# Kernel optimization log

Measured on AMD Instinct MI355X. Metric: run time of the kernel, lower is better.

## Reference

```python
import jax, jax.numpy as jnp
import numpy as np

EPS = float(np.finfo(np.float32).eps)
H = 256          # hidden_size
K = 10           # num_event_types
B, S = 32, 4096  # batch, seq_len


def _linear_params(kw, kb, fan_in, fan_out):
    # torch nn.Linear default init (uniform +-1/sqrt(fan_in)), then abs + clamp(min=eps)
    bound = 1.0 / np.sqrt(fan_in)
    w = jnp.clip(jnp.abs(jax.random.uniform(kw, (fan_out, fan_in), minval=-bound, maxval=bound, dtype=jnp.float32)), EPS)
    b = jnp.clip(jnp.abs(jax.random.uniform(kb, (fan_out,), minval=-bound, maxval=bound, dtype=jnp.float32)), EPS)
    return w, b


def setup_inputs() -> dict:
    key = jax.random.key(0)
    ks = jax.random.split(key, 12)
    w1, b1 = _linear_params(ks[0], ks[1], 1, H)        # layer_dense_1
    w2, b2 = _linear_params(ks[2], ks[3], 2 * H, H)    # layer_dense_2
    wA, bA = _linear_params(ks[4], ks[5], H, H)        # module_list[0]
    wB, bB = _linear_params(ks[6], ks[7], H, H)        # module_list[1]
    w3, b3 = _linear_params(ks[8], ks[9], H, K)        # layer_dense_3 linear
    hidden_states = jax.random.normal(ks[10], (B, S, H), dtype=jnp.float32)
    time_delta_seqs = jax.random.uniform(ks[11], (B, S), dtype=jnp.float32)
    return dict(hidden_states=hidden_states, time_delta_seqs=time_delta_seqs,
                w1=w1, b1=b1, w2=w2, b2=b2, wA=wA, bA=bA, wB=wB, bB=bB, w3=w3, b3=b3)


def _cumul_hazard(td, h, w1, b1, w2, b2, wA, bA, wB, bB, w3, b3):
    # layer_dense_1: Linear(1 -> H) on td[..., None]
    t = td[..., None] * w1[:, 0] + b1                      # [B,S,H]
    out = jnp.tanh(jnp.concatenate([h, t], axis=-1) @ w2.T + b2)  # [B,S,H]
    out = jnp.tanh(out @ wA.T + bA)
    out = jnp.tanh(out @ wB.T + bB)
    return jax.nn.softplus(out @ w3.T + b3)                # [B,S,K]


def reference(hidden_states, time_delta_seqs, w1, b1, w2, b2, wA, bA, wB, bB, w3, b3):
    f = lambda td: _cumul_hazard(td, hidden_states, w1, b1, w2, b2, wA, bA, wB, bB, w3, b3)
    # Each output element depends only on its own t[b,s] (elementwise in time),
    # so a single forward-mode JVP with tangent=ones yields the exact per-element
    # derivative for ALL event types at once (fuses torch's per-type grad loop).
    integral_lambda, d_dt = jax.jvp(f, (time_delta_seqs,), (jnp.ones_like(time_delta_seqs),))
    # torch takes grad of .mean() over [B,S], which scales the derivative by 1/(B*S)
    derivative_integral_lambda = d_dt / time_delta_seqs.size
    return integral_lambda, derivative_integral_lambda
```

## Files before the change

### kernel.cpp

```cpp
#include <hip/hip_runtime.h>
#include <hip/hip_bf16.h>
#include <stdint.h>

typedef __bf16 bf16x8 __attribute__((ext_vector_type(8)));
typedef __bf16 bf16x4 __attribute__((ext_vector_type(4)));
typedef float  f32x4  __attribute__((ext_vector_type(4)));
typedef float  f32x2  __attribute__((ext_vector_type(2)));

#define MFMA16(a,b,c) __builtin_amdgcn_mfma_f32_16x16x32_bf16((a),(b),(c),0,0,0)

static constexpr int H_   = 256;
static constexpr int KEV  = 10;
static constexpr int NTOK = 32 * 4096;

__device__ __forceinline__ float ptanh(float x){
    float t = x * x;
    float n = fmaf(t, t + 105.0f, 945.0f);
    float d = fmaf(t, fmaf(t, 15.0f, 420.0f), 945.0f);
    float r = x * n * __builtin_amdgcn_rcpf(d);
    return __builtin_amdgcn_fmed3f(r, -1.0f, 1.0f);
}

__device__ __forceinline__ bf16x8 cvtFrag(const float* p){
    f32x4 a = *(const f32x4*)p;
    f32x4 b = *(const f32x4*)(p + 4);
    bf16x8 r;
    #pragma unroll
    for (int j = 0; j < 4; ++j){ r[j] = (__bf16)a[j]; r[4 + j] = (__bf16)b[j]; }
    return r;
}

__global__ void prep_vc(const float* __restrict__ w1, const float* __restrict__ b1,
                        const float* __restrict__ w2, const float* __restrict__ b2,
                        const float* __restrict__ b3, float* __restrict__ vc){
    int j = blockIdx.x * 4 + (threadIdx.x >> 6);
    int l = threadIdx.x & 63;
    const float* row = w2 + (size_t)j * (2 * H_) + H_;
    float v = 0.f, cc = 0.f;
    #pragma unroll
    for (int i = 0; i < 4; ++i){
        int k = l + 64 * i;
        float w = row[k];
        v  += w * w1[k];
        cc += w * b1[k];
    }
    #pragma unroll
    for (int off = 32; off; off >>= 1){
        v  += __shfl_down(v,  off, 64);
        cc += __shfl_down(cc, off, 64);
    }
    if (l == 0){ vc[j] = v; vc[H_ + j] = cc + b2[j]; }
    if (blockIdx.x == 0 && threadIdx.x < 16)
        vc[2 * H_ + threadIdx.x] = (threadIdx.x < KEV) ? b3[threadIdx.x] : 0.0f;
}

__global__ void prep_pack(const float* __restrict__ w2, const float* __restrict__ wA,
                          const float* __restrict__ wB, const float* __restrict__ w3,
                          __hip_bfloat16* __restrict__ pk){
    int b  = blockIdx.x;
    int L  = b >> 4, n0 = b & 15;
    const float* W; int K, nrows;
    if (b == 48){ W = w3; K = H_; nrows = KEV; }
    else { W = (L == 0) ? w2 : ((L == 1) ? wA : wB); K = (L == 0) ? 2 * H_ : H_; nrows = 16; }
    __hip_bfloat16* dst = pk + (size_t)b * 4096;
    int t = threadIdx.x;
    #pragma unroll
    for (int u = 0; u < 2; ++u){
        int slot = t * 2 + u;
        int s = slot >> 6, q = (slot >> 4) & 3, c = slot & 15;
        int rr = (b == 48) ? c : (n0 * 16 + c);
        if (c < nrows){
            const float* src = W + (size_t)rr * K + 32 * s + 8 * q;
            #pragma unroll
            for (int j = 0; j < 8; ++j) dst[slot * 8 + j] = __float2bfloat16(src[j]);
        } else {
            #pragma unroll
            for (int j = 0; j < 8; ++j) dst[slot * 8 + j] = __float2bfloat16(0.0f);
        }
    }
}

typedef const __attribute__((address_space(1))) void* gvp;
typedef __attribute__((address_space(3)))       void* lvp;

__device__ __forceinline__ void stage_chunk(const __hip_bfloat16* wpk, __hip_bfloat16* buf,
                                            int g, int wave, int lane){
    const char* src = (const char*)wpk + (size_t)g * 8192 + wave * 2048 + lane * 16;
    char*       dst = (char*)buf + wave * 2048;
    __builtin_amdgcn_global_load_lds((gvp)(const void*)src,          (lvp)(void*)dst,          16, 0, 0);
    __builtin_amdgcn_global_load_lds((gvp)(const void*)(src + 1024), (lvp)(void*)(dst + 1024), 16, 0, 0);
}

__global__ __launch_bounds__(256, 2) void chfn_kernel(
    const float* __restrict__ hs, const float* __restrict__ td,
    const __hip_bfloat16* __restrict__ wpk,
    const float* __restrict__ bA, const float* __restrict__ bB,
    const float* __restrict__ vc,
    float* __restrict__ out)
{
    __shared__ __hip_bfloat16 sW[2 * 4096];
    __shared__ __hip_bfloat16 sA[4 * 16 * H_];
    __shared__ __hip_bfloat16 sD[4 * 16 * H_];

    const int tid  = threadIdx.x;
    const int wave = tid >> 6;
    const int lane = tid & 63;
    const int q    = lane >> 4;
    const int c    = lane & 15;
    const int tb   = blockIdx.x * 64 + wave * 16;
    const int wrow = wave * 16;
    const int xr   = (c >> 1) & 7;
    const int ws   = q * 16 + c;

    stage_chunk(wpk, sW, 0, wave, lane);

    bf16x8 aF[8], aB[8];
    {
        const float* h0 = hs + (size_t)(tb + c) * H_ + 8 * q;
        #pragma unroll
        for (int s = 0; s < 8; ++s) aF[s] = cvtFrag(h0 + 32 * s);
    }
    float myTd = td[tb + c];

    bf16x8 W[8];

    #pragma unroll 2
    for (int n0 = 0; n0 < 16; ++n0){
        __syncthreads();
        stage_chunk(wpk, sW + ((n0 + 1) & 1) * 4096, n0 + 1, wave, lane);
        {
            const bf16x8* b = (const bf16x8*)(sW + (n0 & 1) * 4096) + ws;
            #pragma unroll
            for (int s = 0; s < 8; ++s) W[s] = b[s * 64];
        }
        f32x4 v4 = *(const f32x4*)(vc + n0 * 16 + 4 * q);
        f32x4 c4 = *(const f32x4*)(vc + H_ + n0 * 16 + 4 * q);
        f32x4 fa = c4;
        f32x4 fb = {0.f,0.f,0.f,0.f};
        #pragma unroll
        for (int s = 0; s < 4; ++s){
            fa = MFMA16(W[s],     aF[s],     fa);
            fb = MFMA16(W[s + 4], aF[s + 4], fb);
        }
        bf16x4 pa, pd;
        #pragma unroll
        for (int r = 0; r < 4; ++r){
            float x  = fmaf(myTd, v4[r], fa[r] + fb[r]);
            float th = ptanh(x);
            float dd = fmaf(-th, th, 1.0f) * v4[r];
            pa[r] = (__bf16)th; pd[r] = (__bf16)dd;
        }
        int chn = 2 * n0 + (q >> 1);
        int off = (wrow + c) * H_ + ((((chn + 4 * c) & 31) ^ xr) << 3) + ((q & 1) << 2);
        *(bf16x4*)((void*)(sA + off)) = pa;
        *(bf16x4*)((void*)(sD + off)) = pd;
    }

    #pragma unroll 1
    for (int L = 0; L < 2; ++L){
        const float* bias = L ? bB : bA;
        {
            const __hip_bfloat16* a0 = sA + (wrow + c) * H_;
            const __hip_bfloat16* d0 = sD + (wrow + c) * H_;
            #pragma unroll
            for (int s = 0; s < 8; ++s){
                int g8 = ((((4 * s + q) + 4 * c) & 31) ^ xr) << 3;
                aF[s] = *(const bf16x8*)(a0 + g8);
                aB[s] = *(const bf16x8*)(d0 + g8);
            }
        }
        #pragma unroll 2
        for (int n0 = 0; n0 < 16; ++n0){
            int g = 16 * (L + 1) + n0;
            __syncthreads();
            stage_chunk(wpk, sW + ((g + 1) & 1) * 4096, g + 1, wave, lane);
            {
                const bf16x8* b = (const bf16x8*)(sW + (g & 1) * 4096) + ws;
                #pragma unroll
                for (int s = 0; s < 8; ++s) W[s] = b[s * 64];
            }
            f32x4 b4 = *(const f32x4*)(bias + n0 * 16 + 4 * q);
            f32x4 fa = b4;
            f32x4 fb = {0.f,0.f,0.f,0.f};
            f32x4 ga = {0.f,0.f,0.f,0.f};
            f32x4 gb = {0.f,0.f,0.f,0.f};
            #pragma unroll
            for (int s = 0; s < 4; ++s){
                fa = MFMA16(W[s],     aF[s],     fa);
                ga = MFMA16(W[s],     aB[s],     ga);
                fb = MFMA16(W[s + 4], aF[s + 4], fb);
                gb = MFMA16(W[s + 4], aB[s + 4], gb);
            }
            bf16x4 pa, pd;
            #pragma unroll
            for (int r = 0; r < 4; ++r){
                float th = ptanh(fa[r] + fb[r]);
                float dd = fmaf(-th, th, 1.0f) * (ga[r] + gb[r]);
                pa[r] = (__bf16)th; pd[r] = (__bf16)dd;
            }
            int chn = 2 * n0 + (q >> 1);
            int off = (wrow + c) * H_ + ((((chn + 4 * c) & 31) ^ xr) << 3) + ((q & 1) << 2);
            *(bf16x4*)((void*)(sA + off)) = pa;
            *(bf16x4*)((void*)(sD + off)) = pd;
        }
    }

    {
        __syncthreads();
        {
            const bf16x8* b = (const bf16x8*)sW + ws;
            #pragma unroll
            for (int s = 0; s < 8; ++s) W[s] = b[s * 64];
        }
        const __hip_bfloat16* a0 = sA + (wrow + c) * H_;
        const __hip_bfloat16* d0 = sD + (wrow + c) * H_;
        #pragma unroll
        for (int s = 0; s < 8; ++s){
            int g8 = ((((4 * s + q) + 4 * c) & 31) ^ xr) << 3;
            aF[s] = *(const bf16x8*)(a0 + g8);
            aB[s] = *(const bf16x8*)(d0 + g8);
        }
        f32x4 b4 = *(const f32x4*)(vc + 2 * H_ + 4 * q);
        f32x4 fa = b4;
        f32x4 fb = {0.f,0.f,0.f,0.f};
        f32x4 ga = {0.f,0.f,0.f,0.f};
        f32x4 gb = {0.f,0.f,0.f,0.f};
        #pragma unroll
        for (int s = 0; s < 4; ++s){
            fa = MFMA16(W[s],     aF[s],     fa);
            ga = MFMA16(W[s],     aB[s],     ga);
            fb = MFMA16(W[s + 4], aF[s + 4], fb);
            gb = MFMA16(W[s + 4], aB[s + 4], gb);
        }
        int fbase = 4 * q;
        size_t token = tb + c;
        float sp[4], dv[4];
        #pragma unroll
        for (int r = 0; r < 4; ++r){
            float z  = fa[r] + fb[r];
            float a  = fabsf(z);
            float e  = __builtin_amdgcn_exp2f(-1.4426950408889634f * a);
            sp[r] = fmaxf(z, 0.f) + 0.69314718055994531f * __builtin_amdgcn_logf(1.0f + e);
            float sg = __builtin_amdgcn_rcpf(1.0f + e);
            sg = (z >= 0.f) ? sg : 1.0f - sg;
            dv[r] = sg * (ga[r] + gb[r]) * (1.0f / 131072.0f);
        }
        float* o0 = out + token * KEV + fbase;
        float* o1 = out + (size_t)NTOK * KEV + token * KEV + fbase;
        if (q < 2){
            *(f32x2*)o0       = (f32x2){sp[0], sp[1]};
            *(f32x2*)(o0 + 2) = (f32x2){sp[2], sp[3]};
            *(f32x2*)o1       = (f32x2){dv[0], dv[1]};
            *(f32x2*)(o1 + 2) = (f32x2){dv[2], dv[3]};
        } else if (q == 2){
            *(f32x2*)o0 = (f32x2){sp[0], sp[1]};
            *(f32x2*)o1 = (f32x2){dv[0], dv[1]};
        }
    }
}

extern "C" void kernel_launch(void* const* d_in, const int* in_sizes, int n_in,
                              void* d_out, int out_size, void* d_ws, size_t ws_size,
                              hipStream_t stream){
    const float* hs = (const float*)d_in[0];
    const float* td = (const float*)d_in[1];
    const float* w1 = (const float*)d_in[2];
    const float* b1 = (const float*)d_in[3];
    const float* w2 = (const float*)d_in[4];
    const float* b2 = (const float*)d_in[5];
    const float* wA = (const float*)d_in[6];
    const float* bA = (const float*)d_in[7];
    const float* wB = (const float*)d_in[8];
    const float* bB = (const float*)d_in[9];
    const float* w3 = (const float*)d_in[10];
    const float* b3 = (const float*)d_in[11];

    float*          vc  = (float*)d_ws;
    __hip_bfloat16* wpk = (__hip_bfloat16*)((char*)d_ws + 4096);
    float*          outp = (float*)d_out;

    prep_vc  <<<64, 256, 0, stream>>>(w1, b1, w2, b2, b3, vc);
    prep_pack<<<49, 256, 0, stream>>>(w2, wA, wB, w3, wpk);
    chfn_kernel<<<NTOK / 64, 256, 0, stream>>>(hs, td, wpk, bA, bB, vc, outp);
}
```

Measured before the change: 349.0 us.

## Keep tangent activations in registers via small LDS transpose buffer, raise occupancy

The full-width per-row tangent buffer in LDS is replaced by a small per-wave staging buffer. Each pair of output tiles is transposed through it straight into MFMA B-fragments held in registers (ping-pong TA/TB across layers). This cuts LDS use and per-layer tangent reloads, and launch bounds are raised to three blocks per CU for higher occupancy. Loops are fully unrolled and extra fragment arrays are live, which raises register pressure and risks spills under the tighter register budget.

```diff
diff --git a/kernel.cpp b/kernel.cpp
--- a/kernel.cpp
+++ b/kernel.cpp
@@ -91,7 +91,7 @@
     __builtin_amdgcn_global_load_lds((gvp)(const void*)(src + 1024), (lvp)(void*)(dst + 1024), 16, 0, 0);
 }
 
-__global__ __launch_bounds__(256, 2) void chfn_kernel(
+__global__ __launch_bounds__(256, 3) void chfn_kernel(
     const float* __restrict__ hs, const float* __restrict__ td,
     const __hip_bfloat16* __restrict__ wpk,
     const float* __restrict__ bA, const float* __restrict__ bB,
@@ -100,7 +100,7 @@
 {
     __shared__ __hip_bfloat16 sW[2 * 4096];
     __shared__ __hip_bfloat16 sA[4 * 16 * H_];
-    __shared__ __hip_bfloat16 sD[4 * 16 * H_];
+    __shared__ __hip_bfloat16 sT[4 * 512];
 
     const int tid  = threadIdx.x;
     const int wave = tid >> 6;
@@ -110,11 +110,14 @@
     const int tb   = blockIdx.x * 64 + wave * 16;
     const int wrow = wave * 16;
     const int xr   = (c >> 1) & 7;
+    const int sx   = (c >> 1) & 1;
     const int ws   = q * 16 + c;
+    const int e0w  = wave * 512 + 32 * c + 4 * q;
+    const int r0w  = wave * 512 + 32 * c + ((8 * q) ^ (sx << 4));
 
     stage_chunk(wpk, sW, 0, wave, lane);
 
-    bf16x8 aF[8], aB[8];
+    bf16x8 aF[8], TA[8], TB[8];
     {
         const float* h0 = hs + (size_t)(tb + c) * H_ + 8 * q;
         #pragma unroll
@@ -122,103 +125,109 @@
     }
     float myTd = td[tb + c];
 
-    bf16x8 W[8];
-
-    #pragma unroll 2
-    for (int n0 = 0; n0 < 16; ++n0){
-        __syncthreads();
-        stage_chunk(wpk, sW + ((n0 + 1) & 1) * 4096, n0 + 1, wave, lane);
-        {
-            const bf16x8* b = (const bf16x8*)(sW + (n0 & 1) * 4096) + ws;
-            #pragma unroll
-            for (int s = 0; s < 8; ++s) W[s] = b[s * 64];
-        }
-        f32x4 v4 = *(const f32x4*)(vc + n0 * 16 + 4 * q);
-        f32x4 c4 = *(const f32x4*)(vc + H_ + n0 * 16 + 4 * q);
-        f32x4 fa = c4;
-        f32x4 fb = {0.f,0.f,0.f,0.f};
-        #pragma unroll
-        for (int s = 0; s < 4; ++s){
-            fa = MFMA16(W[s],     aF[s],     fa);
-            fb = MFMA16(W[s + 4], aF[s + 4], fb);
-        }
-        bf16x4 pa, pd;
-        #pragma unroll
-        for (int r = 0; r < 4; ++r){
-            float x  = fmaf(myTd, v4[r], fa[r] + fb[r]);
-            float th = ptanh(x);
-            float dd = fmaf(-th, th, 1.0f) * v4[r];
-            pa[r] = (__bf16)th; pd[r] = (__bf16)dd;
-        }
-        int chn = 2 * n0 + (q >> 1);
-        int off = (wrow + c) * H_ + ((((chn + 4 * c) & 31) ^ xr) << 3) + ((q & 1) << 2);
-        *(bf16x4*)((void*)(sA + off)) = pa;
-        *(bf16x4*)((void*)(sD + off)) = pd;
-    }
-
-    #pragma unroll 1
-    for (int L = 0; L < 2; ++L){
-        const float* bias = L ? bB : bA;
+    #pragma unroll
+    for (int jj = 0; jj < 8; ++jj){
+        #pragma unroll
+        for (int t = 0; t < 2; ++t){
+            int n0 = 2 * jj + t;
+            __syncthreads();
+            stage_chunk(wpk, sW + ((n0 + 1) & 1) * 4096, n0 + 1, wave, lane);
+            bf16x8 W[8];
+            {   const bf16x8* b = (const bf16x8*)(sW + (n0 & 1) * 4096) + ws;
+                #pragma unroll
+                for (int s = 0; s < 8; ++s) W[s] = b[s * 64];
+            }
+            f32x4 v4 = *(const f32x4*)(vc + n0 * 16 + 4 * q);
+            f32x4 c4 = *(const f32x4*)(vc + H_ + n0 * 16 + 4 * q);
+            f32x4 fa = c4;
+            f32x4 fb = {0.f,0.f,0.f,0.f};
+            #pragma unroll
+            for (int s = 0; s < 4; ++s){
+                fa = MFMA16(W[s],     aF[s],     fa);
+                fb = MFMA16(W[s + 4], aF[s + 4], fb);
+            }
+            bf16x4 pa, pd;
+            #pragma unroll
+            for (int r = 0; r < 4; ++r){
+                float x  = fmaf(myTd, v4[r], fa[r] + fb[r]);
+                float th = ptanh(x);
+                float dd = fmaf(-th, th, 1.0f) * v4[r];
+                pa[r] = (__bf16)th; pd[r] = (__bf16)dd;
+            }
+            int chn = 2 * n0 + (q >> 1);
+            int off = (wrow + c) * H_ + ((((chn + 4 * c) & 31) ^ xr) << 3) + ((q & 1) << 2);
+            *(bf16x4*)((void*)(sA + off)) = pa;
+            *(bf16x4*)((void*)(sT + e0w + ((t ^ sx) << 4))) = pd;
+        }
+        TB[jj] = *(const bf16x8*)(sT + r0w);
+    }
+
+    auto run_layer = [&](const float* __restrict__ bias, int g0,
+                         bf16x8 (&Tin)[8], bf16x8 (&Tout)[8]){
         {
             const __hip_bfloat16* a0 = sA + (wrow + c) * H_;
-            const __hip_bfloat16* d0 = sD + (wrow + c) * H_;
             #pragma unroll
             for (int s = 0; s < 8; ++s){
                 int g8 = ((((4 * s + q) + 4 * c) & 31) ^ xr) << 3;
                 aF[s] = *(const bf16x8*)(a0 + g8);
-                aB[s] = *(const bf16x8*)(d0 + g8);
-            }
-        }
-        #pragma unroll 2
-        for (int n0 = 0; n0 < 16; ++n0){
-            int g = 16 * (L + 1) + n0;
-            __syncthreads();
-            stage_chunk(wpk, sW + ((g + 1) & 1) * 4096, g + 1, wave, lane);
-            {
-                const bf16x8* b = (const bf16x8*)(sW + (g & 1) * 4096) + ws;
+            }
+        }
+        #pragma unroll
+        for (int jj = 0; jj < 8; ++jj){
+            #pragma unroll
+            for (int t = 0; t < 2; ++t){
+                int n0 = 2 * jj + t;
+                int g  = g0 + n0;
+                __syncthreads();
+                stage_chunk(wpk, sW + ((g + 1) & 1) * 4096, g + 1, wave, lane);
+                bf16x8 W[8];
+                {   const bf16x8* b = (const bf16x8*)(sW + (g & 1) * 4096) + ws;
+                    #pragma unroll
+                    for (int s = 0; s < 8; ++s) W[s] = b[s * 64];
+                }
+                f32x4 b4 = *(const f32x4*)(bias + n0 * 16 + 4 * q);
+                f32x4 fa = b4;
+                f32x4 fb = {0.f,0.f,0.f,0.f};
+                f32x4 ga = {0.f,0.f,0.f,0.f};
+                f32x4 gb = {0.f,0.f,0.f,0.f};
                 #pragma unroll
-                for (int s = 0; s < 8; ++s) W[s] = b[s * 64];
-            }
-            f32x4 b4 = *(const f32x4*)(bias + n0 * 16 + 4 * q);
-            f32x4 fa = b4;
-            f32x4 fb = {0.f,0.f,0.f,0.f};
-            f32x4 ga = {0.f,0.f,0.f,0.f};
-            f32x4 gb = {0.f,0.f,0.f,0.f};
-            #pragma unroll
-            for (int s = 0; s < 4; ++s){
-                fa = MFMA16(W[s],     aF[s],     fa);
-                ga = MFMA16(W[s],     aB[s],     ga);
-                fb = MFMA16(W[s + 4], aF[s + 4], fb);
-                gb = MFMA16(W[s + 4], aB[s + 4], gb);
-            }
-            bf16x4 pa, pd;
-            #pragma unroll
-            for (int r = 0; r < 4; ++r){
-                float th = ptanh(fa[r] + fb[r]);
-                float dd = fmaf(-th, th, 1.0f) * (ga[r] + gb[r]);
-                pa[r] = (__bf16)th; pd[r] = (__bf16)dd;
-            }
-            int chn = 2 * n0 + (q >> 1);
-            int off = (wrow + c) * H_ + ((((chn + 4 * c) & 31) ^ xr) << 3) + ((q & 1) << 2);
-            *(bf16x4*)((void*)(sA + off)) = pa;
-            *(bf16x4*)((void*)(sD + off)) = pd;
-        }
-    }
+                for (int s = 0; s < 4; ++s){
+                    fa = MFMA16(W[s],     aF[s],      fa);
+                    ga = MFMA16(W[s],     Tin[s],     ga);
+                    fb = MFMA16(W[s + 4], aF[s + 4],  fb);
+                    gb = MFMA16(W[s + 4], Tin[s + 4], gb);
+                }
+                bf16x4 pa, pd;
+                #pragma unroll
+                for (int r = 0; r < 4; ++r){
+                    float th = ptanh(fa[r] + fb[r]);
+                    float dd = fmaf(-th, th, 1.0f) * (ga[r] + gb[r]);
+                    pa[r] = (__bf16)th; pd[r] = (__bf16)dd;
+                }
+                int chn = 2 * n0 + (q >> 1);
+                int off = (wrow + c) * H_ + ((((chn + 4 * c) & 31) ^ xr) << 3) + ((q & 1) << 2);
+                *(bf16x4*)((void*)(sA + off)) = pa;
+                *(bf16x4*)((void*)(sT + e0w + ((t ^ sx) << 4))) = pd;
+            }
+            Tout[jj] = *(const bf16x8*)(sT + r0w);
+        }
+    };
+
+    run_layer(bA, 16, TB, TA);
+    run_layer(bB, 32, TA, TB);
 
     {
         __syncthreads();
-        {
-            const bf16x8* b = (const bf16x8*)sW + ws;
+        bf16x8 W[8];
+        {   const bf16x8* b = (const bf16x8*)sW + ws;
             #pragma unroll
             for (int s = 0; s < 8; ++s) W[s] = b[s * 64];
         }
         const __hip_bfloat16* a0 = sA + (wrow + c) * H_;
-        const __hip_bfloat16* d0 = sD + (wrow + c) * H_;
         #pragma unroll
         for (int s = 0; s < 8; ++s){
             int g8 = ((((4 * s + q) + 4 * c) & 31) ^ xr) << 3;
             aF[s] = *(const bf16x8*)(a0 + g8);
-            aB[s] = *(const bf16x8*)(d0 + g8);
         }
         f32x4 b4 = *(const f32x4*)(vc + 2 * H_ + 4 * q);
         f32x4 fa = b4;
@@ -228,9 +237,9 @@
         #pragma unroll
         for (int s = 0; s < 4; ++s){
             fa = MFMA16(W[s],     aF[s],     fa);
-            ga = MFMA16(W[s],     aB[s],     ga);
+            ga = MFMA16(W[s],     TB[s],     ga);
             fb = MFMA16(W[s + 4], aF[s + 4], fb);
-            gb = MFMA16(W[s + 4], aB[s + 4], gb);
+            gb = MFMA16(W[s + 4], TB[s + 4], gb);
         }
         int fbase = 4 * q;
         size_t token = tb + c;
```

Measured after the change: 317.4 us. 9.1% less time.
